# Kernel tuning notes

Hardware: AMD Instinct MI355X
Metric: run time of the kernel (lower is better)

Reference implementation:

```python
import jax, jax.numpy as jnp
import numpy as np

N_NODES = 50000
N_EDGES = 600000
FEAT = 128
N_LAYERS = 4


def setup_inputs() -> dict:
    key = jax.random.key(0)
    ks = jax.random.split(key, 7)
    feats = jax.random.normal(ks[0], (N_NODES, FEAT), dtype=jnp.float32)
    src = jax.random.randint(ks[1], (N_EDGES,), 0, N_NODES)
    dst = jax.random.randint(ks[2], (N_EDGES,), 0, N_NODES)
    s = 1.0 / np.sqrt(FEAT)  # torch Linear default init range
    theta_w = jax.random.uniform(ks[3], (N_LAYERS, FEAT, FEAT), jnp.float32, -s, s)
    theta_b = jax.random.uniform(ks[4], (N_LAYERS, FEAT), jnp.float32, -s, s)
    phi_w = jax.random.uniform(ks[5], (N_LAYERS, FEAT, FEAT), jnp.float32, -s, s)
    phi_b = jax.random.uniform(ks[6], (N_LAYERS, FEAT), jnp.float32, -s, s)
    return {"feats": feats, "src": src, "dst": dst,
            "theta_w": theta_w, "theta_b": theta_b,
            "phi_w": phi_w, "phi_b": phi_b}


def _edgeconv(x, src, dst, tw, tb, pw, pb):
    # EdgeConv (Wang et al. 2018): out_i = max_{(j->i) in E} theta(x_j - x_i) + phi(x_i)
    phi = x @ pw.T + pb                       # [N, F] node-level linear (avoid per-edge recompute)
    diff = x[src] - x[dst]                    # [E, F] gather
    msg = diff @ tw.T + tb + phi[dst]         # [E, F]
    agg = jax.ops.segment_max(msg, dst, num_segments=x.shape[0])  # [N, F]
    # nodes with no incoming edges get -inf from segment_max; zero them (DGL convention)
    return jnp.where(jnp.isneginf(agg), jnp.zeros_like(agg), agg)


def reference(feats, src, dst, theta_w, theta_b, phi_w, phi_b):
    x = feats
    for l in range(N_LAYERS):
        x = _edgeconv(x, src, dst, theta_w[l], theta_b[l], phi_w[l], phi_b[l])
        x = jax.nn.relu(x)
    return x
```

## Files before the change

### kernel.cpp

```cpp
#include <hip/hip_runtime.h>

#define FEAT 128
#define SLABS 4

typedef __attribute__((ext_vector_type(8))) _Float16 f16x8;
typedef __attribute__((ext_vector_type(2))) _Float16 f16x2;
typedef __attribute__((ext_vector_type(4))) float f32x4;

static __device__ __forceinline__ int wave_incl_scan(int v, int lane) {
#pragma unroll
    for (int off = 1; off < 64; off <<= 1) {
        int u = __shfl_up(v, off, 64);
        if (lane >= off) v += u;
    }
    return v;
}


__global__ void prep_kernel(const int* __restrict__ src, const int* __restrict__ dst,
                            int* __restrict__ deg4, int* __restrict__ erank,
                            int E, int slab_size,
                            const float* __restrict__ tw, const float* __restrict__ pw,
                            const float* __restrict__ tb, const float* __restrict__ pb,
                            _Float16* __restrict__ wt, _Float16* __restrict__ wp,
                            float* __restrict__ bsum, int wn, int nbias,
                            const float* __restrict__ x, _Float16* __restrict__ x16, int xn4,
                            int hb, int wb) {
    int bid = blockIdx.x;
    if (bid < hb) {
        int e = bid * 256 + threadIdx.x;
        if (e < E) {
            int sl = src[e] / slab_size;
            erank[e] = atomicAdd(&deg4[dst[e] * SLABS + sl], 1);
        }
    } else if (bid < hb + wb) {
        int i = (bid - hb) * 256 + threadIdx.x;
        if (i < wn) { wt[i] = (_Float16)tw[i]; wp[i] = (_Float16)pw[i]; }
        if (i < nbias) bsum[i] = tb[i] + pb[i];
    } else {
        int i = (bid - hb - wb) * 256 + threadIdx.x;
        if (i < xn4) {
            float4 v = ((const float4*)x)[i];
            f16x2 a, b;
            a[0] = (_Float16)v.x; a[1] = (_Float16)v.y;
            b[0] = (_Float16)v.z; b[1] = (_Float16)v.w;
            ((f16x2*)x16)[i * 2] = a;
            ((f16x2*)x16)[i * 2 + 1] = b;
        }
    }
}


__global__ __launch_bounds__(1024) void scan1_kernel(const int* __restrict__ deg,
                                                     int* __restrict__ row_ptr,
                                                     int* __restrict__ bsum, int N4) {
    int i = blockIdx.x * 1024 + threadIdx.x;
    int lane = threadIdx.x & 63;
    int w = threadIdx.x >> 6;
    int v = (i < N4) ? deg[i] : 0;
    int inc = wave_incl_scan(v, lane);
    __shared__ int wsum[16];
    if (lane == 63) wsum[w] = inc;
    __syncthreads();
    if (w == 0) {
        int s = (lane < 16) ? wsum[lane] : 0;
        int si = wave_incl_scan(s, lane);
        if (lane < 16) wsum[lane] = si - s;
    }
    __syncthreads();
    int exc = inc - v + wsum[w];
    if (i < N4) row_ptr[i] = exc;
    if (threadIdx.x == 1023) bsum[blockIdx.x] = exc + v;
}

__global__ __launch_bounds__(1024) void scan2_kernel(const int* __restrict__ bsum,
                                                     int* __restrict__ boff,
                                                     int* __restrict__ row_ptr,
                                                     int nb, int N4, int E) {
    int tid = threadIdx.x;
    int lane = tid & 63;
    int w = tid >> 6;
    int v = (tid < nb) ? bsum[tid] : 0;
    int inc = wave_incl_scan(v, lane);
    __shared__ int wsum[16];
    if (lane == 63) wsum[w] = inc;
    __syncthreads();
    if (w == 0) {
        int s = (lane < 16) ? wsum[lane] : 0;
        int si = wave_incl_scan(s, lane);
        if (lane < 16) wsum[lane] = si - s;
    }
    __syncthreads();
    int b = inc - v + wsum[w];
    if (tid <= nb) boff[tid] = b;
    if (tid == (N4 >> 10)) row_ptr[N4] = E - b;
}


static __device__ __forceinline__ void gemm_body(
        int bx, int nslab,
        const _Float16* __restrict__ x16,
        const _Float16* __restrict__ wt, const _Float16* __restrict__ wp,
        const float* __restrict__ bias,
        _Float16* __restrict__ t16, _Float16* __restrict__ q16, int M) {
    int lane = threadIdx.x & 63;
    int l16 = lane & 15;
    int quad = lane >> 4;
    int cn0 = (threadIdx.x >> 6) * 32;

    f16x8 bt[2][4], bp[2][4];
    float biasv[2];
#pragma unroll
    for (int ct = 0; ct < 2; ++ct) {
        int col = cn0 + ct * 16 + l16;
        biasv[ct] = bias[col];
#pragma unroll
        for (int kk = 0; kk < 4; ++kk) {
            int k = kk * 32 + quad * 8;
            bt[ct][kk] = *(const f16x8*)(wt + (size_t)col * FEAT + k);
            bp[ct][kk] = *(const f16x8*)(wp + (size_t)col * FEAT + k);
        }
    }

    int rbase0 = bx * (nslab * 16);
#pragma unroll 1
    for (int rs = 0; rs < nslab; ++rs) {
        int rbase = rbase0 + rs * 16;
        int row = rbase + l16;
        int rowc = (row < M) ? row : (M - 1);
        f16x8 a[4];
#pragma unroll
        for (int kk = 0; kk < 4; ++kk)
            a[kk] = *(const f16x8*)(x16 + (size_t)rowc * FEAT + kk * 32 + quad * 8);

        f32x4 accT[2] = {{0.f, 0.f, 0.f, 0.f}, {0.f, 0.f, 0.f, 0.f}};
        f32x4 accP[2] = {{0.f, 0.f, 0.f, 0.f}, {0.f, 0.f, 0.f, 0.f}};
#pragma unroll
        for (int kk = 0; kk < 4; ++kk) {
#pragma unroll
            for (int ct = 0; ct < 2; ++ct) {
                accT[ct] = __builtin_amdgcn_mfma_f32_16x16x32_f16(a[kk], bt[ct][kk], accT[ct], 0, 0, 0);
                accP[ct] = __builtin_amdgcn_mfma_f32_16x16x32_f16(a[kk], bp[ct][kk], accP[ct], 0, 0, 0);
            }
        }
#pragma unroll
        for (int ct = 0; ct < 2; ++ct) {
            int col = cn0 + ct * 16 + l16;
#pragma unroll
            for (int r = 0; r < 4; ++r) {
                int ro = rbase + quad * 4 + r;
                if (ro < M) {
                    t16[(size_t)ro * FEAT + col] = (_Float16)accT[ct][r];
                    q16[(size_t)ro * FEAT + col] =
                        (_Float16)(accP[ct][r] - accT[ct][r] + biasv[ct]);
                }
            }
        }
    }
}

__global__ __launch_bounds__(256) void fused0_kernel(
        const _Float16* __restrict__ x16,
        const _Float16* __restrict__ wt, const _Float16* __restrict__ wp,
        const float* __restrict__ bias,
        _Float16* __restrict__ t16, _Float16* __restrict__ q16, int M, int gb,
        const int* __restrict__ src, const int* __restrict__ dst,
        const int* __restrict__ row_ptr4, const int* __restrict__ boff,
        const int* __restrict__ erank,
        int* __restrict__ esrc, int E, int slab_size) {
    if ((int)blockIdx.x < gb) {
        gemm_body(blockIdx.x, 8, x16, wt, wp, bias, t16, q16, M);
    } else {
        int e = (blockIdx.x - gb) * 256 + threadIdx.x;
        if (e < E) {
            int s = src[e];
            int key = dst[e] * SLABS + s / slab_size;
            esrc[row_ptr4[key] + boff[key >> 10] + erank[e]] = s;
        }
    }
}


static __device__ __forceinline__ f16x8 vmax8(f16x8 a, f16x8 b) {
#pragma unroll
    for (int i = 0; i < 8; ++i) a[i] = (a[i] > b[i]) ? a[i] : b[i];
    return a;
}

static __device__ __forceinline__ f16x8 shfl_xor8(f16x8 v, int m) {
    union { f16x8 h; int i[4]; } u, r;
    u.h = v;
#pragma unroll
    for (int d = 0; d < 4; ++d) r.i[d] = __shfl_xor(u.i[d], m, 64);
    return r.h;
}

static __device__ __forceinline__ f16x8 gather_max(
        const _Float16* __restrict__ t16, const int* __restrict__ esrc,
        int beg, int cnt, int lane, int g, int c) {
    const _Float16 NEGINF = (_Float16)(-65504.0f);
    f16x8 m0, m1;
#pragma unroll
    for (int i = 0; i < 8; ++i) { m0[i] = NEGINF; m1[i] = NEGINF; }

    for (int cb = 0; cb < cnt; cb += 64) {
        int lim = cnt - cb; if (lim > 64) lim = 64;
        int a = beg + cb + (lane < lim ? lane : 0);
        int myidx = esrc[a];
        for (int base = 0; base < lim; base += 8) {
            int e0 = base + g;     if (e0 >= lim) e0 = 0;
            int e1 = base + 4 + g; if (e1 >= lim) e1 = 0;
            int i0 = __shfl(myidx, e0, 64);
            int i1 = __shfl(myidx, e1, 64);
            f16x8 v0 = *(const f16x8*)(t16 + (size_t)i0 * FEAT + c * 8);
            f16x8 v1 = *(const f16x8*)(t16 + (size_t)i1 * FEAT + c * 8);
            m0 = vmax8(m0, v0);
            m1 = vmax8(m1, v1);
        }
    }

    f16x8 mm = vmax8(m0, m1);
    mm = vmax8(mm, shfl_xor8(mm, 16));
    mm = vmax8(mm, shfl_xor8(mm, 32));
    return mm;
}

static __device__ __forceinline__ f16x2 slot_pair(f16x8 mm, int g) {
    union { f16x8 h; int i[4]; } um; um.h = mm;
    int w01 = (g & 1) ? um.i[1] : um.i[0];
    int w23 = (g & 1) ? um.i[3] : um.i[2];
    int w = (g & 2) ? w23 : w01;
    union { int i; f16x2 h; } uw; uw.i = w;
    return uw.h;
}


__global__ __launch_bounds__(256) void fusedagg_kernel(
        const _Float16* __restrict__ t16, const _Float16* __restrict__ q16,
        const int* __restrict__ row_ptr4, const int* __restrict__ boff,
        const int* __restrict__ esrc,
        const _Float16* __restrict__ wt, const _Float16* __restrict__ wp,
        const float* __restrict__ bias,
        _Float16* __restrict__ tn, _Float16* __restrict__ qn, int N) {
    __shared__ _Float16 xl[16 * FEAT];
    int wv = threadIdx.x >> 6;
    int lane = threadIdx.x & 63;
    int g = lane >> 4;
    int c = lane & 15;
    int node0 = blockIdx.x * 16;

#pragma unroll 1
    for (int k = 0; k < 4; ++k) {
        int nr = wv * 4 + k;
        int node = node0 + nr;
        float o0 = 0.f, o1 = 0.f;
        if (node < N) {
            int bi = node * SLABS;
            int beg = row_ptr4[bi] + boff[bi >> 10];
            int end = row_ptr4[bi + SLABS] + boff[(bi + SLABS) >> 10];
            f16x2 qv = *(const f16x2*)(q16 + (size_t)node * FEAT + c * 8 + g * 2);
            f16x8 mm = gather_max(t16, esrc, beg, end - beg, lane, g, c);
            f16x2 mp = slot_pair(mm, g);
            o0 = fmaxf((float)mp[0] + (float)qv[0], 0.f);
            o1 = fmaxf((float)mp[1] + (float)qv[1], 0.f);
        }
        f16x2 oh; oh[0] = (_Float16)o0; oh[1] = (_Float16)o1;
        int byteoff = (nr * 256 + c * 16 + g * 4) ^ ((nr & 7) << 4);
        *(f16x2*)((char*)xl + byteoff) = oh;
    }
    __syncthreads();

    int l16 = lane & 15;
    int quad = lane >> 4;
    int cn0 = wv * 32;
    f16x8 a[4];
#pragma unroll
    for (int kk = 0; kk < 4; ++kk) {
        int byteoff = (l16 * 256 + kk * 64 + quad * 16) ^ ((l16 & 7) << 4);
        a[kk] = *(const f16x8*)((const char*)xl + byteoff);
    }
#pragma unroll 1
    for (int ct = 0; ct < 2; ++ct) {
        int col = cn0 + ct * 16 + l16;
        float bv = bias[col];
        f16x8 fb[4];
#pragma unroll
        for (int kk = 0; kk < 4; ++kk)
            fb[kk] = *(const f16x8*)(wt + (size_t)col * FEAT + kk * 32 + quad * 8);
        f32x4 accT = {0.f, 0.f, 0.f, 0.f};
#pragma unroll
        for (int kk = 0; kk < 4; ++kk)
            accT = __builtin_amdgcn_mfma_f32_16x16x32_f16(a[kk], fb[kk], accT, 0, 0, 0);
#pragma unroll
        for (int kk = 0; kk < 4; ++kk)
            fb[kk] = *(const f16x8*)(wp + (size_t)col * FEAT + kk * 32 + quad * 8);
        f32x4 accP = {0.f, 0.f, 0.f, 0.f};
#pragma unroll
        for (int kk = 0; kk < 4; ++kk)
            accP = __builtin_amdgcn_mfma_f32_16x16x32_f16(a[kk], fb[kk], accP, 0, 0, 0);
#pragma unroll
        for (int r = 0; r < 4; ++r) {
            int ro = node0 + quad * 4 + r;
            if (ro < N) {
                tn[(size_t)ro * FEAT + col] = (_Float16)accT[r];
                qn[(size_t)ro * FEAT + col] = (_Float16)(accP[r] - accT[r] + bv);
            }
        }
    }
}

__global__ __launch_bounds__(256) void agg_kernel(
        const _Float16* __restrict__ t16, const _Float16* __restrict__ q16,
        const int* __restrict__ row_ptr4, const int* __restrict__ boff,
        const int* __restrict__ esrc,
        float* __restrict__ outf, int N) {
    int wv = threadIdx.x >> 6;
    int lane = threadIdx.x & 63;
    int node = blockIdx.x * 4 + wv;
    if (node >= N) return;

    int g = lane >> 4;
    int c = lane & 15;

    int bi = node * SLABS;
    int beg = row_ptr4[bi] + boff[bi >> 10];
    int end = row_ptr4[bi + SLABS] + boff[(bi + SLABS) >> 10];

    f16x2 qv = *(const f16x2*)(q16 + (size_t)node * FEAT + c * 8 + g * 2);
    f16x8 mm = gather_max(t16, esrc, beg, end - beg, lane, g, c);
    f16x2 mp = slot_pair(mm, g);

    float o0 = fmaxf((float)mp[0] + (float)qv[0], 0.f);
    float o1 = fmaxf((float)mp[1] + (float)qv[1], 0.f);
    float2 ov = make_float2(o0, o1);
    *(float2*)(outf + (size_t)node * FEAT + c * 8 + g * 2) = ov;
}


extern "C" void kernel_launch(void* const* d_in, const int* in_sizes, int n_in,
                              void* d_out, int out_size, void* d_ws, size_t ws_size,
                              hipStream_t stream) {
    const float* feats   = (const float*)d_in[0];
    const int*   src     = (const int*)d_in[1];
    const int*   dst     = (const int*)d_in[2];
    const float* theta_w = (const float*)d_in[3];
    const float* theta_b = (const float*)d_in[4];
    const float* phi_w   = (const float*)d_in[5];
    const float* phi_b   = (const float*)d_in[6];

    const int N = in_sizes[0] / FEAT;
    const int E = in_sizes[1];
    const int L = in_sizes[3] / (FEAT * FEAT);
    const int N4 = N * SLABS;
    const int slab_size = (N + SLABS - 1) / SLABS;

    char* ws = (char*)d_ws;
    size_t off = 0;
    auto alloc = [&](size_t bytes) -> void* {
        void* ptr = ws + off;
        off = (off + bytes + 255) & ~(size_t)255;
        return ptr;
    };
    _Float16* tbuf[2];
    _Float16* qbuf[2];
    tbuf[0] = (_Float16*)alloc((size_t)N * FEAT * 2);
    tbuf[1] = (_Float16*)alloc((size_t)N * FEAT * 2);
    qbuf[0] = (_Float16*)alloc((size_t)N * FEAT * 2);
    qbuf[1] = (_Float16*)alloc((size_t)N * FEAT * 2);
    _Float16* x16 = (_Float16*)alloc((size_t)N * FEAT * 2);
    _Float16* wt16 = (_Float16*)alloc((size_t)L * FEAT * FEAT * 2);
    _Float16* wp16 = (_Float16*)alloc((size_t)L * FEAT * FEAT * 2);
    float* bsum_b = (float*)alloc((size_t)L * FEAT * sizeof(float));
    int* deg4     = (int*)alloc((size_t)N4 * sizeof(int));
    int* row_ptr4 = (int*)alloc((size_t)(N4 + 1) * sizeof(int));
    int* erank    = (int*)alloc((size_t)E * sizeof(int));
    int* esrc     = (int*)alloc((size_t)E * sizeof(int));
    int* bsum     = (int*)alloc(2048 * sizeof(int));
    int* boff     = (int*)alloc(2048 * sizeof(int));
    (void)ws_size;

    hipMemsetAsync(deg4, 0, (size_t)N4 * sizeof(int), stream);

    int eb = (E + 255) / 256;
    int wn = L * FEAT * FEAT;
    int wb = (wn + 255) / 256;
    int xn4 = N * FEAT / 4;
    int xb = (xn4 + 255) / 256;
    prep_kernel<<<eb + wb + xb, 256, 0, stream>>>(
        src, dst, deg4, erank, E, slab_size,
        theta_w, phi_w, theta_b, phi_b, wt16, wp16, bsum_b, wn, L * FEAT,
        feats, x16, xn4, eb, wb);

    int nb = (N4 + 1023) >> 10;
    scan1_kernel<<<nb, 1024, 0, stream>>>(deg4, row_ptr4, bsum, N4);
    scan2_kernel<<<1, 1024, 0, stream>>>(bsum, boff, row_ptr4, nb, N4, E);

    int gb = (N + 127) / 128;
    fused0_kernel<<<gb + eb, 256, 0, stream>>>(
        x16, wt16, wp16, bsum_b, tbuf[0], qbuf[0], N, gb,
        src, dst, row_ptr4, boff, erank, esrc, E, slab_size);

    int fb = (N + 15) / 16;
    for (int l = 0; l + 1 < L; ++l) {
        fusedagg_kernel<<<fb, 256, 0, stream>>>(
            tbuf[l & 1], qbuf[l & 1], row_ptr4, boff, esrc,
            wt16 + (size_t)(l + 1) * FEAT * FEAT,
            wp16 + (size_t)(l + 1) * FEAT * FEAT,
            bsum_b + (size_t)(l + 1) * FEAT,
            tbuf[(l + 1) & 1], qbuf[(l + 1) & 1], N);
    }

    int ab = (N + 3) / 4;
    agg_kernel<<<ab, 256, 0, stream>>>(
        tbuf[(L - 1) & 1], qbuf[(L - 1) & 1], row_ptr4, boff, esrc,
        (float*)d_out, N);
}
```

Measured before the change: 310.8 us.

## Drop source-slab CSR sorting and fuse feature fp16 conversion into first GEMM

Removes the 4-way source-slab sub-bucketing of the CSR, so edges are grouped only by destination. This shrinks the degree and row-pointer arrays and the scan work, at the cost of losing the source locality the slabs gave to the gathers. It also drops the separate fp32-to-fp16 pass over the input features and converts them inside the first-layer GEMM loads. That saves one full read and write of the feature matrix, but the GEMM now reads twice the bytes per row.

```diff
diff --git a/kernel.cpp b/kernel.cpp
--- a/kernel.cpp
+++ b/kernel.cpp
@@ -1,7 +1,6 @@
 #include <hip/hip_runtime.h>
 
 #define FEAT 128
-#define SLABS 4
 
 typedef __attribute__((ext_vector_type(8))) _Float16 f16x8;
 typedef __attribute__((ext_vector_type(2))) _Float16 f16x2;
@@ -18,46 +17,33 @@
 
 
 __global__ void prep_kernel(const int* __restrict__ src, const int* __restrict__ dst,
-                            int* __restrict__ deg4, int* __restrict__ erank,
-                            int E, int slab_size,
+                            int* __restrict__ deg, int* __restrict__ erank, int E,
                             const float* __restrict__ tw, const float* __restrict__ pw,
                             const float* __restrict__ tb, const float* __restrict__ pb,
                             _Float16* __restrict__ wt, _Float16* __restrict__ wp,
                             float* __restrict__ bsum, int wn, int nbias,
-                            const float* __restrict__ x, _Float16* __restrict__ x16, int xn4,
-                            int hb, int wb) {
+                            int hb) {
     int bid = blockIdx.x;
     if (bid < hb) {
         int e = bid * 256 + threadIdx.x;
         if (e < E) {
-            int sl = src[e] / slab_size;
-            erank[e] = atomicAdd(&deg4[dst[e] * SLABS + sl], 1);
-        }
-    } else if (bid < hb + wb) {
+            erank[e] = atomicAdd(&deg[dst[e]], 1);
+        }
+    } else {
         int i = (bid - hb) * 256 + threadIdx.x;
         if (i < wn) { wt[i] = (_Float16)tw[i]; wp[i] = (_Float16)pw[i]; }
         if (i < nbias) bsum[i] = tb[i] + pb[i];
-    } else {
-        int i = (bid - hb - wb) * 256 + threadIdx.x;
-        if (i < xn4) {
-            float4 v = ((const float4*)x)[i];
-            f16x2 a, b;
-            a[0] = (_Float16)v.x; a[1] = (_Float16)v.y;
-            b[0] = (_Float16)v.z; b[1] = (_Float16)v.w;
-            ((f16x2*)x16)[i * 2] = a;
-            ((f16x2*)x16)[i * 2 + 1] = b;
-        }
     }
 }
 
 
 __global__ __launch_bounds__(1024) void scan1_kernel(const int* __restrict__ deg,
                                                      int* __restrict__ row_ptr,
-                                                     int* __restrict__ bsum, int N4) {
+                                                     int* __restrict__ bsum, int N) {
     int i = blockIdx.x * 1024 + threadIdx.x;
     int lane = threadIdx.x & 63;
     int w = threadIdx.x >> 6;
-    int v = (i < N4) ? deg[i] : 0;
+    int v = (i < N) ? deg[i] : 0;
     int inc = wave_incl_scan(v, lane);
     __shared__ int wsum[16];
     if (lane == 63) wsum[w] = inc;
@@ -69,14 +55,14 @@
     }
     __syncthreads();
     int exc = inc - v + wsum[w];
-    if (i < N4) row_ptr[i] = exc;
+    if (i < N) row_ptr[i] = exc;
     if (threadIdx.x == 1023) bsum[blockIdx.x] = exc + v;
 }
 
 __global__ __launch_bounds__(1024) void scan2_kernel(const int* __restrict__ bsum,
                                                      int* __restrict__ boff,
                                                      int* __restrict__ row_ptr,
-                                                     int nb, int N4, int E) {
+                                                     int nb, int N, int E) {
     int tid = threadIdx.x;
     int lane = tid & 63;
     int w = tid >> 6;
@@ -93,89 +79,87 @@
     __syncthreads();
     int b = inc - v + wsum[w];
     if (tid <= nb) boff[tid] = b;
-    if (tid == (N4 >> 10)) row_ptr[N4] = E - b;
-}
-
-
-static __device__ __forceinline__ void gemm_body(
-        int bx, int nslab,
-        const _Float16* __restrict__ x16,
-        const _Float16* __restrict__ wt, const _Float16* __restrict__ wp,
-        const float* __restrict__ bias,
-        _Float16* __restrict__ t16, _Float16* __restrict__ q16, int M) {
-    int lane = threadIdx.x & 63;
-    int l16 = lane & 15;
-    int quad = lane >> 4;
-    int cn0 = (threadIdx.x >> 6) * 32;
-
-    f16x8 bt[2][4], bp[2][4];
-    float biasv[2];
-#pragma unroll
-    for (int ct = 0; ct < 2; ++ct) {
-        int col = cn0 + ct * 16 + l16;
-        biasv[ct] = bias[col];
-#pragma unroll
-        for (int kk = 0; kk < 4; ++kk) {
-            int k = kk * 32 + quad * 8;
-            bt[ct][kk] = *(const f16x8*)(wt + (size_t)col * FEAT + k);
-            bp[ct][kk] = *(const f16x8*)(wp + (size_t)col * FEAT + k);
-        }
-    }
-
-    int rbase0 = bx * (nslab * 16);
-#pragma unroll 1
-    for (int rs = 0; rs < nslab; ++rs) {
-        int rbase = rbase0 + rs * 16;
-        int row = rbase + l16;
-        int rowc = (row < M) ? row : (M - 1);
-        f16x8 a[4];
-#pragma unroll
-        for (int kk = 0; kk < 4; ++kk)
-            a[kk] = *(const f16x8*)(x16 + (size_t)rowc * FEAT + kk * 32 + quad * 8);
-
-        f32x4 accT[2] = {{0.f, 0.f, 0.f, 0.f}, {0.f, 0.f, 0.f, 0.f}};
-        f32x4 accP[2] = {{0.f, 0.f, 0.f, 0.f}, {0.f, 0.f, 0.f, 0.f}};
-#pragma unroll
-        for (int kk = 0; kk < 4; ++kk) {
-#pragma unroll
-            for (int ct = 0; ct < 2; ++ct) {
-                accT[ct] = __builtin_amdgcn_mfma_f32_16x16x32_f16(a[kk], bt[ct][kk], accT[ct], 0, 0, 0);
-                accP[ct] = __builtin_amdgcn_mfma_f32_16x16x32_f16(a[kk], bp[ct][kk], accP[ct], 0, 0, 0);
-            }
-        }
-#pragma unroll
-        for (int ct = 0; ct < 2; ++ct) {
-            int col = cn0 + ct * 16 + l16;
-#pragma unroll
-            for (int r = 0; r < 4; ++r) {
-                int ro = rbase + quad * 4 + r;
-                if (ro < M) {
-                    t16[(size_t)ro * FEAT + col] = (_Float16)accT[ct][r];
-                    q16[(size_t)ro * FEAT + col] =
-                        (_Float16)(accP[ct][r] - accT[ct][r] + biasv[ct]);
-                }
-            }
-        }
-    }
-}
+    if (tid == (N >> 10)) row_ptr[N] = E - b;
+}
+
 
 __global__ __launch_bounds__(256) void fused0_kernel(
-        const _Float16* __restrict__ x16,
+        const float* __restrict__ xf,
         const _Float16* __restrict__ wt, const _Float16* __restrict__ wp,
         const float* __restrict__ bias,
         _Float16* __restrict__ t16, _Float16* __restrict__ q16, int M, int gb,
         const int* __restrict__ src, const int* __restrict__ dst,
-        const int* __restrict__ row_ptr4, const int* __restrict__ boff,
+        const int* __restrict__ row_ptr, const int* __restrict__ boff,
         const int* __restrict__ erank,
-        int* __restrict__ esrc, int E, int slab_size) {
+        int* __restrict__ esrc, int E) {
     if ((int)blockIdx.x < gb) {
-        gemm_body(blockIdx.x, 8, x16, wt, wp, bias, t16, q16, M);
+        int lane = threadIdx.x & 63;
+        int l16 = lane & 15;
+        int quad = lane >> 4;
+        int cn0 = (threadIdx.x >> 6) * 32;
+
+        f16x8 bt[2][4], bp[2][4];
+        float biasv[2];
+#pragma unroll
+        for (int ct = 0; ct < 2; ++ct) {
+            int col = cn0 + ct * 16 + l16;
+            biasv[ct] = bias[col];
+#pragma unroll
+            for (int kk = 0; kk < 4; ++kk) {
+                int k = kk * 32 + quad * 8;
+                bt[ct][kk] = *(const f16x8*)(wt + (size_t)col * FEAT + k);
+                bp[ct][kk] = *(const f16x8*)(wp + (size_t)col * FEAT + k);
+            }
+        }
+
+        int rbase0 = blockIdx.x * 128;
+#pragma unroll 1
+        for (int rs = 0; rs < 8; ++rs) {
+            int rbase = rbase0 + rs * 16;
+            int row = rbase + l16;
+            int rowc = (row < M) ? row : (M - 1);
+            f16x8 a[4];
+#pragma unroll
+            for (int kk = 0; kk < 4; ++kk) {
+                const float4* p = (const float4*)(xf + (size_t)rowc * FEAT + kk * 32 + quad * 8);
+                float4 v0 = p[0], v1 = p[1];
+                f16x8 aa;
+                aa[0] = (_Float16)v0.x; aa[1] = (_Float16)v0.y;
+                aa[2] = (_Float16)v0.z; aa[3] = (_Float16)v0.w;
+                aa[4] = (_Float16)v1.x; aa[5] = (_Float16)v1.y;
+                aa[6] = (_Float16)v1.z; aa[7] = (_Float16)v1.w;
+                a[kk] = aa;
+            }
+
+            f32x4 accT[2] = {{0.f, 0.f, 0.f, 0.f}, {0.f, 0.f, 0.f, 0.f}};
+            f32x4 accP[2] = {{0.f, 0.f, 0.f, 0.f}, {0.f, 0.f, 0.f, 0.f}};
+#pragma unroll
+            for (int kk = 0; kk < 4; ++kk) {
+#pragma unroll
+                for (int ct = 0; ct < 2; ++ct) {
+                    accT[ct] = __builtin_amdgcn_mfma_f32_16x16x32_f16(a[kk], bt[ct][kk], accT[ct], 0, 0, 0);
+                    accP[ct] = __builtin_amdgcn_mfma_f32_16x16x32_f16(a[kk], bp[ct][kk], accP[ct], 0, 0, 0);
+                }
+            }
+#pragma unroll
+            for (int ct = 0; ct < 2; ++ct) {
+                int col = cn0 + ct * 16 + l16;
+#pragma unroll
+                for (int r = 0; r < 4; ++r) {
+                    int ro = rbase + quad * 4 + r;
+                    if (ro < M) {
+                        t16[(size_t)ro * FEAT + col] = (_Float16)accT[ct][r];
+                        q16[(size_t)ro * FEAT + col] =
+                            (_Float16)(accP[ct][r] - accT[ct][r] + biasv[ct]);
+                    }
+                }
+            }
+        }
     } else {
         int e = (blockIdx.x - gb) * 256 + threadIdx.x;
         if (e < E) {
-            int s = src[e];
-            int key = dst[e] * SLABS + s / slab_size;
-            esrc[row_ptr4[key] + boff[key >> 10] + erank[e]] = s;
+            int key = dst[e];
+            esrc[row_ptr[key] + boff[key >> 10] + erank[e]] = src[e];
         }
     }
 }
@@ -237,7 +221,7 @@
 
 __global__ __launch_bounds__(256) void fusedagg_kernel(
         const _Float16* __restrict__ t16, const _Float16* __restrict__ q16,
-        const int* __restrict__ row_ptr4, const int* __restrict__ boff,
+        const int* __restrict__ row_ptr, const int* __restrict__ boff,
         const int* __restrict__ esrc,
         const _Float16* __restrict__ wt, const _Float16* __restrict__ wp,
         const float* __restrict__ bias,
@@ -255,9 +239,8 @@
         int node = node0 + nr;
         float o0 = 0.f, o1 = 0.f;
         if (node < N) {
-            int bi = node * SLABS;
-            int beg = row_ptr4[bi] + boff[bi >> 10];
-            int end = row_ptr4[bi + SLABS] + boff[(bi + SLABS) >> 10];
+            int beg = row_ptr[node] + boff[node >> 10];
+            int end = row_ptr[node + 1] + boff[(node + 1) >> 10];
             f16x2 qv = *(const f16x2*)(q16 + (size_t)node * FEAT + c * 8 + g * 2);
             f16x8 mm = gather_max(t16, esrc, beg, end - beg, lane, g, c);
             f16x2 mp = slot_pair(mm, g);
@@ -311,7 +294,7 @@
 
 __global__ __launch_bounds__(256) void agg_kernel(
         const _Float16* __restrict__ t16, const _Float16* __restrict__ q16,
-        const int* __restrict__ row_ptr4, const int* __restrict__ boff,
+        const int* __restrict__ row_ptr, const int* __restrict__ boff,
         const int* __restrict__ esrc,
         float* __restrict__ outf, int N) {
     int wv = threadIdx.x >> 6;
@@ -322,9 +305,8 @@
     int g = lane >> 4;
     int c = lane & 15;
 
-    int bi = node * SLABS;
-    int beg = row_ptr4[bi] + boff[bi >> 10];
-    int end = row_ptr4[bi + SLABS] + boff[(bi + SLABS) >> 10];
+    int beg = row_ptr[node] + boff[node >> 10];
+    int end = row_ptr[node + 1] + boff[(node + 1) >> 10];
 
     f16x2 qv = *(const f16x2*)(q16 + (size_t)node * FEAT + c * 8 + g * 2);
     f16x8 mm = gather_max(t16, esrc, beg, end - beg, lane, g, c);
@@ -351,8 +333,6 @@
     const int N = in_sizes[0] / FEAT;
     const int E = in_sizes[1];
     const int L = in_sizes[3] / (FEAT * FEAT);
-    const int N4 = N * SLABS;
-    const int slab_size = (N + SLABS - 1) / SLABS;
 
     char* ws = (char*)d_ws;
     size_t off = 0;
@@ -367,43 +347,40 @@
     tbuf[1] = (_Float16*)alloc((size_t)N * FEAT * 2);
     qbuf[0] = (_Float16*)alloc((size_t)N * FEAT * 2);
     qbuf[1] = (_Float16*)alloc((size_t)N * FEAT * 2);
-    _Float16* x16 = (_Float16*)alloc((size_t)N * FEAT * 2);
     _Float16* wt16 = (_Float16*)alloc((size_t)L * FEAT * FEAT * 2);
     _Float16* wp16 = (_Float16*)alloc((size_t)L * FEAT * FEAT * 2);
     float* bsum_b = (float*)alloc((size_t)L * FEAT * sizeof(float));
-    int* deg4     = (int*)alloc((size_t)N4 * sizeof(int));
-    int* row_ptr4 = (int*)alloc((size_t)(N4 + 1) * sizeof(int));
+    int* deg      = (int*)alloc((size_t)N * sizeof(int));
+    int* row_ptr  = (int*)alloc((size_t)(N + 1) * sizeof(int));
     int* erank    = (int*)alloc((size_t)E * sizeof(int));
     int* esrc     = (int*)alloc((size_t)E * sizeof(int));
     int* bsum     = (int*)alloc(2048 * sizeof(int));
     int* boff     = (int*)alloc(2048 * sizeof(int));
     (void)ws_size;
 
-    hipMemsetAsync(deg4, 0, (size_t)N4 * sizeof(int), stream);
+    hipMemsetAsync(deg, 0, (size_t)N * sizeof(int), stream);
 
     int eb = (E + 255) / 256;
     int wn = L * FEAT * FEAT;
     int wb = (wn + 255) / 256;
-    int xn4 = N * FEAT / 4;
-    int xb = (xn4 + 255) / 256;
-    prep_kernel<<<eb + wb + xb, 256, 0, stream>>>(
-        src, dst, deg4, erank, E, slab_size,
+    prep_kernel<<<eb + wb, 256, 0, stream>>>(
+        src, dst, deg, erank, E,
         theta_w, phi_w, theta_b, phi_b, wt16, wp16, bsum_b, wn, L * FEAT,
-        feats, x16, xn4, eb, wb);
-
-    int nb = (N4 + 1023) >> 10;
-    scan1_kernel<<<nb, 1024, 0, stream>>>(deg4, row_ptr4, bsum, N4);
-    scan2_kernel<<<1, 1024, 0, stream>>>(bsum, boff, row_ptr4, nb, N4, E);
+        eb);
+
+    int nb = (N + 1023) >> 10;
+    scan1_kernel<<<nb, 1024, 0, stream>>>(deg, row_ptr, bsum, N);
+    scan2_kernel<<<1, 1024, 0, stream>>>(bsum, boff, row_ptr, nb, N, E);
 
     int gb = (N + 127) / 128;
     fused0_kernel<<<gb + eb, 256, 0, stream>>>(
-        x16, wt16, wp16, bsum_b, tbuf[0], qbuf[0], N, gb,
-        src, dst, row_ptr4, boff, erank, esrc, E, slab_size);
+        feats, wt16, wp16, bsum_b, tbuf[0], qbuf[0], N, gb,
+        src, dst, row_ptr, boff, erank, esrc, E);
 
     int fb = (N + 15) / 16;
     for (int l = 0; l + 1 < L; ++l) {
         fusedagg_kernel<<<fb, 256, 0, stream>>>(
-            tbuf[l & 1], qbuf[l & 1], row_ptr4, boff, esrc,
+            tbuf[l & 1], qbuf[l & 1], row_ptr, boff, esrc,
             wt16 + (size_t)(l + 1) * FEAT * FEAT,
             wp16 + (size_t)(l + 1) * FEAT * FEAT,
             bsum_b + (size_t)(l + 1) * FEAT,
@@ -412,6 +389,6 @@
 
     int ab = (N + 3) / 4;
     agg_kernel<<<ab, 256, 0, stream>>>(
-        tbuf[(L - 1) & 1], qbuf[(L - 1) & 1], row_ptr4, boff, esrc,
+        tbuf[(L - 1) & 1], qbuf[(L - 1) & 1], row_ptr, boff, esrc,
         (float*)d_out, N);
 }
```

After: 325.2 us. +4.6%, slower.
